# Optimization experiments

Measured on AMD Instinct MI355X. Metric: run time of the kernel, lower is better.

The kernel has to match this reference:

```python
import jax, jax.numpy as jnp
import numpy as np

B, P, K_NB, D, H = 4, 1024, 32, 768, 12
S = P + 1
HD = D // H  # 64

def _ln(x, w, b):
    m = jnp.mean(x, -1, keepdims=True)
    v = jnp.var(x, -1, keepdims=True)
    return (x - m) / jnp.sqrt(v + 1e-5) * w + b

def setup_inputs() -> dict:
    key = jax.random.key(0)
    ks = jax.random.split(key, 8)
    w = lambda k, sh: jax.random.normal(k, sh, jnp.float32) * 0.02
    return {
        'x': jax.random.normal(ks[0], (B, S, D), jnp.float32),
        'routes': jax.random.randint(ks[1], (P, K_NB), 0, P, dtype=jnp.int32),
        'qkv_w': w(ks[2], (D, 3 * D)), 'qkv_b': jnp.zeros((3 * D,), jnp.float32),
        'proj_w': w(ks[3], (D, D)), 'proj_b': jnp.zeros((D,), jnp.float32),
        'ln1_w': jnp.ones((D,), jnp.float32), 'ln1_b': jnp.zeros((D,), jnp.float32),
        'ln2_w': jnp.ones((D,), jnp.float32), 'ln2_b': jnp.zeros((D,), jnp.float32),
        'mlp_w1': w(ks[4], (D, 4 * D)), 'mlp_b1': jnp.zeros((4 * D,), jnp.float32),
        'mlp_w2': w(ks[5], (4 * D, D)), 'mlp_b2': jnp.zeros((D,), jnp.float32),
    }

def reference(x, routes, qkv_w, qkv_b, proj_w, proj_b, ln1_w, ln1_b,
              ln2_w, ln2_b, mlp_w1, mlp_b1, mlp_w2, mlp_b2):
    scale = HD ** -0.5
    xn = _ln(x, ln1_w, ln1_b)
    qkv = (xn @ qkv_w + qkv_b).reshape(B, S, 3, H, HD).transpose(2, 0, 3, 1, 4)
    Q, Kt, V = qkv[0], qkv[1], qkv[2]  # each [B,H,S,HD]
    # CLS token: full dense attention over all S tokens
    sc = jnp.einsum('bhqd,bhkd->bhqk', Q[:, :, :1], Kt) * scale
    oc = jnp.einsum('bhqk,bhkd->bhqd', jax.nn.softmax(sc, -1), V)  # [B,H,1,HD]
    # patch tokens: sparse attention over k routed neighbors
    r = routes + 1  # shift past CLS (buffer routes_shifted)
    Kg = Kt[:, :, r, :]  # [B,H,P,k,HD] gathered keys
    Vg = V[:, :, r, :]   # [B,H,P,k,HD] gathered values
    sp = jnp.einsum('bhpd,bhpkd->bhpk', Q[:, :, 1:], Kg) * scale
    op = jnp.einsum('bhpk,bhpkd->bhpd', jax.nn.softmax(sp, -1), Vg)
    out = jnp.concatenate([oc, op], axis=2).transpose(0, 2, 1, 3).reshape(B, S, D)
    x = x + (out @ proj_w + proj_b)
    h = _ln(x, ln2_w, ln2_b)
    h = jax.nn.gelu(h @ mlp_w1 + mlp_b1, approximate=False) @ mlp_w2 + mlp_b2
    return x + h
```

## Files before the change

### kernel.cpp

```cpp
#include <hip/hip_runtime.h>
#include <hip/hip_bf16.h>

using bf16 = __hip_bfloat16;
using s8v  = __attribute__((ext_vector_type(8))) short;
using f4v  = __attribute__((ext_vector_type(4))) float;

constexpr int B_   = 4;
constexpr int P_   = 1024;
constexpr int KNB  = 32;
constexpr int D_   = 768;
constexpr int H_   = 12;
constexpr int S_   = P_ + 1;
constexpr int M_   = B_ * S_;
constexpr int MPAD = 4224;

#define DEVI static __device__ __forceinline__
#define WAITVM(N) asm volatile("s_waitcnt vmcnt(" #N ")" ::: "memory")
#define MEMFENCE  asm volatile("" ::: "memory")

DEVI float b2f_lo(unsigned u) { return __builtin_bit_cast(float, u << 16); }
DEVI float b2f_hi(unsigned u) { return __builtin_bit_cast(float, u & 0xffff0000u); }
DEVI unsigned short f2bu(float f) {
  return __builtin_bit_cast(unsigned short, __float2bfloat16(f));
}

template<int KK, int NN>
__global__ __launch_bounds__(256)
void wt_conv(const float* __restrict__ W, bf16* __restrict__ Wt) {
  __shared__ float t[32][33];
  int bk = blockIdx.x * 32, bn = blockIdx.y * 32;
  int tx = threadIdx.x & 31, ty = threadIdx.x >> 5;
#pragma unroll
  for (int i = 0; i < 32; i += 8)
    t[ty + i][tx] = W[(size_t)(bk + ty + i) * NN + bn + tx];
  __syncthreads();
#pragma unroll
  for (int i = 0; i < 32; i += 8)
    Wt[(size_t)(bn + ty + i) * KK + bk + tx] = __float2bfloat16(t[tx][ty + i]);
}

__global__ __launch_bounds__(256)
void ln_kernel(const float* __restrict__ x, const float* __restrict__ w,
               const float* __restrict__ b, bf16* __restrict__ out) {
  int row = blockIdx.x;
  const float* xr = x + (size_t)row * D_;
  int t = threadIdx.x;
  float v0 = xr[t], v1 = xr[t + 256], v2 = xr[t + 512];
  float s = v0 + v1 + v2;
  float ss = v0 * v0 + v1 * v1 + v2 * v2;
#pragma unroll
  for (int o = 32; o; o >>= 1) { s += __shfl_xor(s, o); ss += __shfl_xor(ss, o); }
  __shared__ float sm[4], sv[4];
  if ((t & 63) == 0) { sm[t >> 6] = s; sv[t >> 6] = ss; }
  __syncthreads();
  float S = sm[0] + sm[1] + sm[2] + sm[3];
  float SS = sv[0] + sv[1] + sv[2] + sv[3];
  float mean = S * (1.f / D_);
  float var  = SS * (1.f / D_) - mean * mean;
  float inv  = rsqrtf(var + 1e-5f);
  bf16* orow = out + (size_t)row * D_;
  orow[t]       = __float2bfloat16((v0 - mean) * inv * w[t]       + b[t]);
  orow[t + 256] = __float2bfloat16((v1 - mean) * inv * w[t + 256] + b[t + 256]);
  orow[t + 512] = __float2bfloat16((v2 - mean) * inv * w[t + 512] + b[t + 512]);
}

template<int BM, int N, int K, int MODE>
__global__ __launch_bounds__(256)
void gemm_bf16(const bf16* __restrict__ A, const bf16* __restrict__ Bt,
               const float* __restrict__ bias, const float* __restrict__ resid,
               void* __restrict__ dst) {
  constexpr int MR   = BM / 32;
  constexpr int LPS  = BM / 64 + 2;
  constexpr int TN   = N / 128;
  constexpr int NBLK = (MPAD / BM) * TN;
  __shared__ bf16 ldsA[4][BM * 32];
  __shared__ bf16 ldsB[4][128 * 32];

  int bid = blockIdx.x;
  constexpr int NQ = NBLK >> 3, NR = NBLK & 7;
  int xcd = bid & 7, off = bid >> 3;
  int swz = (xcd < NR ? xcd * (NQ + 1) : NR * (NQ + 1) + (xcd - NR) * NQ) + off;
  const int tm = swz / TN, tn = swz % TN;

  const int tid = threadIdx.x;
  const int wid = tid >> 6, lane = tid & 63;
  const int wr = wid >> 1, wc = wid & 1;

  auto stage = [&](int bufi, int step) {
    const int k0 = step * 32;
#pragma unroll
    for (int i = 0; i < BM / 64; ++i) {
      int c = wid * 64 + i * 256 + lane;
      int r = c >> 2, slot = c & 3;
      int gs = slot ^ ((r >> 1) & 3);
      const bf16* ga = A + (size_t)(tm * BM + r) * K + k0 + gs * 8;
      bf16* la = &ldsA[bufi][(wid * 64 + i * 256) * 8];
      __builtin_amdgcn_global_load_lds(
          (__attribute__((address_space(1))) void*)ga,
          (__attribute__((address_space(3))) void*)la, 16, 0, 0);
    }
#pragma unroll
    for (int i = 0; i < 2; ++i) {
      int c = wid * 64 + i * 256 + lane;
      int r = c >> 2, slot = c & 3;
      int gs = slot ^ ((r >> 1) & 3);
      const bf16* ga = Bt + (size_t)(tn * 128 + r) * K + k0 + gs * 8;
      bf16* la = &ldsB[bufi][(wid * 64 + i * 256) * 8];
      __builtin_amdgcn_global_load_lds(
          (__attribute__((address_space(1))) void*)ga,
          (__attribute__((address_space(3))) void*)la, 16, 0, 0);
    }
  };

  f4v acc[MR][4] = {};
  const int nk = K / 32;

  stage(0, 0); stage(1, 1); stage(2, 2);

#pragma unroll 4
  for (int kt = 0; kt < nk; ++kt) {
    const int rem = nk - kt;
    if (rem > 2) {
      if constexpr (LPS == 4) WAITVM(8); else WAITVM(6);
    } else if (rem == 2) {
      if constexpr (LPS == 4) WAITVM(4); else WAITVM(3);
    } else {
      WAITVM(0);
    }
    __builtin_amdgcn_s_barrier();
    MEMFENCE;
    if (kt + 3 < nk) stage((kt + 3) & 3, kt + 3);

    const int cur = kt & 3;
    s8v af[MR], bfv[4];
#pragma unroll
    for (int m = 0; m < MR; ++m) {
      int row = wr * (MR * 16) + m * 16 + (lane & 15);
      int slot = (lane >> 4) ^ ((row >> 1) & 3);
      af[m] = *(const s8v*)&ldsA[cur][row * 32 + slot * 8];
    }
#pragma unroll
    for (int n = 0; n < 4; ++n) {
      int row = wc * 64 + n * 16 + (lane & 15);
      int slot = (lane >> 4) ^ ((row >> 1) & 3);
      bfv[n] = *(const s8v*)&ldsB[cur][row * 32 + slot * 8];
    }
#pragma unroll
    for (int m = 0; m < MR; ++m)
#pragma unroll
      for (int n = 0; n < 4; ++n)
        acc[m][n] = __builtin_amdgcn_mfma_f32_16x16x32_bf16(af[m], bfv[n], acc[m][n], 0, 0, 0);
  }

#pragma unroll
  for (int m = 0; m < MR; ++m)
#pragma unroll
    for (int n = 0; n < 4; ++n)
#pragma unroll
      for (int j = 0; j < 4; ++j) {
        int row = tm * BM + wr * (MR * 16) + m * 16 + (lane >> 4) * 4 + j;
        int col = tn * 128 + wc * 64 + n * 16 + (lane & 15);
        float v = acc[m][n][j];
        if (MODE == 0) {
          if (row < M_) {
            float val = v + bias[col];
            int which = col / 768, rem2 = col % 768;
            int bb = row / S_, s = row % S_;
            ((bf16*)dst)[((size_t)(which * B_ + bb) * S_ + s) * 768 + rem2] =
                __float2bfloat16(val);
          }
        } else if (MODE == 1) {
          if (row < M_) {
            float val = v + bias[col] + resid[(size_t)row * N + col];
            ((float*)dst)[(size_t)row * N + col] = val;
          }
        } else {
          float val = v + bias[col];
          val = 0.5f * val * (1.f + erff(val * 0.70710678f));
          ((bf16*)dst)[(size_t)row * N + col] = __float2bfloat16(val);
        }
      }
}

__global__ __launch_bounds__(256)
void cls_partial(const bf16* __restrict__ QKV, float* __restrict__ part) {
  int bh = blockIdx.x, c = blockIdx.y;
  int b = bh / H_, h = bh % H_;
  const bf16* q  = QKV + ((size_t)(0 * B_ + b) * S_) * D_ + h * 64;
  const bf16* Kr = QKV + ((size_t)(1 * B_ + b) * S_) * D_ + h * 64;
  const bf16* Vr = QKV + ((size_t)(2 * B_ + b) * S_) * D_ + h * 64;
  int k0 = c * 256, kn = (c == 3) ? 257 : 256;
  __shared__ float qf[64];
  __shared__ float sc[257];
  __shared__ float red[4];
  __shared__ float pv[4][64];
  int t = threadIdx.x;
  if (t < 64) qf[t] = __bfloat162float(q[t]);
  __syncthreads();
  for (int kk = t; kk < kn; kk += 256) {
    const uint4* k4 = (const uint4*)(Kr + (size_t)(k0 + kk) * D_);
    float s = 0.f;
#pragma unroll
    for (int i = 0; i < 8; ++i) {
      uint4 kv = k4[i];
      const float* q8 = &qf[i * 8];
      s += b2f_lo(kv.x) * q8[0] + b2f_hi(kv.x) * q8[1]
         + b2f_lo(kv.y) * q8[2] + b2f_hi(kv.y) * q8[3]
         + b2f_lo(kv.z) * q8[4] + b2f_hi(kv.z) * q8[5]
         + b2f_lo(kv.w) * q8[6] + b2f_hi(kv.w) * q8[7];
    }
    sc[kk] = s * 0.125f;
  }
  __syncthreads();
  float mx = -1e30f;
  for (int kk = t; kk < kn; kk += 256) mx = fmaxf(mx, sc[kk]);
#pragma unroll
  for (int o = 32; o; o >>= 1) mx = fmaxf(mx, __shfl_xor(mx, o));
  if ((t & 63) == 0) red[t >> 6] = mx;
  __syncthreads();
  float M = fmaxf(fmaxf(red[0], red[1]), fmaxf(red[2], red[3]));
  __syncthreads();
  float sum = 0.f;
  for (int kk = t; kk < kn; kk += 256) { float e = __expf(sc[kk] - M); sc[kk] = e; sum += e; }
#pragma unroll
  for (int o = 32; o; o >>= 1) sum += __shfl_xor(sum, o);
  if ((t & 63) == 0) red[t >> 6] = sum;
  __syncthreads();
  float L = red[0] + red[1] + red[2] + red[3];
  int d = t & 63, kg = t >> 6;
  float acc = 0.f;
  for (int kk = kg; kk < kn; kk += 4)
    acc += sc[kk] * __bfloat162float(Vr[(size_t)(k0 + kk) * D_ + d]);
  pv[kg][d] = acc;
  __syncthreads();
  float* pp = part + ((size_t)bh * 4 + c) * 68;
  if (t < 64) pp[4 + t] = pv[0][t] + pv[1][t] + pv[2][t] + pv[3][t];
  else if (t == 64) pp[0] = M;
  else if (t == 65) pp[1] = L;
}

__global__ __launch_bounds__(64)
void cls_combine(const float* __restrict__ part, bf16* __restrict__ out) {
  int bh = blockIdx.x, t = threadIdx.x;
  const float* pp = part + (size_t)bh * 4 * 68;
  float m0 = pp[0], m1 = pp[68], m2 = pp[136], m3 = pp[204];
  float M = fmaxf(fmaxf(m0, m1), fmaxf(m2, m3));
  float e0 = __expf(m0 - M), e1 = __expf(m1 - M), e2 = __expf(m2 - M), e3 = __expf(m3 - M);
  float L = pp[1] * e0 + pp[69] * e1 + pp[137] * e2 + pp[205] * e3;
  float o = pp[4 + t] * e0 + pp[72 + t] * e1 + pp[140 + t] * e2 + pp[208 + t] * e3;
  int b = bh / H_, h = bh % H_;
  out[(size_t)(b * S_) * D_ + h * 64 + t] = __float2bfloat16(o / L);
}

__global__ __launch_bounds__(256)
void routed_attn(const bf16* __restrict__ QKV, const int* __restrict__ routes,
                 bf16* __restrict__ out) {
  int unit = blockIdx.x * 4 + (threadIdx.x >> 6);
  int lane = threadIdx.x & 63;
  int h = unit % H_;
  int bp = unit / H_;
  int p = bp % P_, b = bp / P_;

  int k = lane & 31, hi = lane >> 5;
  int r = routes[p * KNB + k] + 1;

  const bf16* Qp = QKV + ((size_t)(0 * B_ + b) * S_ + (p + 1)) * D_ + h * 64 + hi * 32;
  const bf16* Kb = QKV + ((size_t)(1 * B_ + b) * S_) * D_;
  const bf16* Vb = QKV + ((size_t)(2 * B_ + b) * S_) * D_;

  const uint4* q4 = (const uint4*)Qp;
  const uint4* k4 = (const uint4*)(Kb + (size_t)r * D_ + h * 64 + hi * 32);
  float dot = 0.f;
#pragma unroll
  for (int i = 0; i < 4; ++i) {
    uint4 qv = q4[i], kv = k4[i];
    dot += b2f_lo(kv.x) * b2f_lo(qv.x) + b2f_hi(kv.x) * b2f_hi(qv.x)
         + b2f_lo(kv.y) * b2f_lo(qv.y) + b2f_hi(kv.y) * b2f_hi(qv.y)
         + b2f_lo(kv.z) * b2f_lo(qv.z) + b2f_hi(kv.z) * b2f_hi(qv.z)
         + b2f_lo(kv.w) * b2f_lo(qv.w) + b2f_hi(kv.w) * b2f_hi(qv.w);
  }
  dot += __shfl_xor(dot, 32);
  float sc = dot * 0.125f;

  float mx = sc;
#pragma unroll
  for (int o = 16; o; o >>= 1) mx = fmaxf(mx, __shfl_xor(mx, o));
  float w = __expf(sc - mx);
  float sum = w;
#pragma unroll
  for (int o = 16; o; o >>= 1) sum += __shfl_xor(sum, o);
  float inv = 1.f / sum;

  int c = lane & 7, kr0 = lane >> 3;
  float acc[8] = {};
#pragma unroll
  for (int j = 0; j < 4; ++j) {
    int kj = (kr0 & 7) + 8 * j;
    float wj = __shfl(w, kj);
    int rj = __shfl(r, kj);
    uint4 vv = *(const uint4*)(Vb + (size_t)rj * D_ + h * 64 + c * 8);
    acc[0] += wj * b2f_lo(vv.x); acc[1] += wj * b2f_hi(vv.x);
    acc[2] += wj * b2f_lo(vv.y); acc[3] += wj * b2f_hi(vv.y);
    acc[4] += wj * b2f_lo(vv.z); acc[5] += wj * b2f_hi(vv.z);
    acc[6] += wj * b2f_lo(vv.w); acc[7] += wj * b2f_hi(vv.w);
  }
#pragma unroll
  for (int s = 8; s < 64; s <<= 1)
#pragma unroll
    for (int d = 0; d < 8; ++d) acc[d] += __shfl_xor(acc[d], s);

  if (lane < 8) {
    s8v o;
#pragma unroll
    for (int d = 0; d < 8; ++d) o[d] = (short)f2bu(acc[d] * inv);
    *(s8v*)(out + ((size_t)(b * S_ + p + 1)) * D_ + h * 64 + c * 8) = o;
  }
}

extern "C" void kernel_launch(void* const* d_in, const int* in_sizes, int n_in,
                              void* d_out, int out_size, void* d_ws, size_t ws_size,
                              hipStream_t stream) {
  const float* x      = (const float*)d_in[0];
  const int*   routes = (const int*)d_in[1];
  const float* qkv_w  = (const float*)d_in[2];
  const float* qkv_b  = (const float*)d_in[3];
  const float* proj_w = (const float*)d_in[4];
  const float* proj_b = (const float*)d_in[5];
  const float* ln1_w  = (const float*)d_in[6];
  const float* ln1_b  = (const float*)d_in[7];
  const float* ln2_w  = (const float*)d_in[8];
  const float* ln2_b  = (const float*)d_in[9];
  const float* mlp_w1 = (const float*)d_in[10];
  const float* mlp_b1 = (const float*)d_in[11];
  const float* mlp_w2 = (const float*)d_in[12];
  const float* mlp_b2 = (const float*)d_in[13];
  float* out = (float*)d_out;

  bf16* qkvw_t  = (bf16*)d_ws;
  bf16* projw_t = qkvw_t + 2304 * 768;
  bf16* mlpw1_t = projw_t + 768 * 768;
  bf16* mlpw2_t = mlpw1_t + 3072 * 768;
  bf16* xnA     = mlpw2_t + 768 * 3072;
  bf16* qkvbuf  = xnA + (size_t)MPAD * 768;
  bf16* attn    = qkvbuf + (size_t)3 * B_ * S_ * 768;
  bf16* h2      = attn + (size_t)MPAD * 768;
  bf16* g       = xnA;
  float* clsp   = (float*)(attn + (size_t)M_ * 768);

  wt_conv<768, 2304><<<dim3(24, 72), 256, 0, stream>>>(qkv_w, qkvw_t);
  wt_conv<768, 768><<<dim3(24, 24), 256, 0, stream>>>(proj_w, projw_t);
  wt_conv<768, 3072><<<dim3(24, 96), 256, 0, stream>>>(mlp_w1, mlpw1_t);
  wt_conv<3072, 768><<<dim3(96, 24), 256, 0, stream>>>(mlp_w2, mlpw2_t);

  ln_kernel<<<M_, 256, 0, stream>>>(x, ln1_w, ln1_b, xnA);

  gemm_bf16<128, 2304, 768, 0><<<33 * 18, 256, 0, stream>>>(xnA, qkvw_t, qkv_b, nullptr, qkvbuf);

  routed_attn<<<(B_ * P_ * H_) / 4, 256, 0, stream>>>(qkvbuf, routes, attn);
  cls_partial<<<dim3(B_ * H_, 4), 256, 0, stream>>>(qkvbuf, clsp);
  cls_combine<<<B_ * H_, 64, 0, stream>>>(clsp, attn);

  gemm_bf16<64, 768, 768, 1><<<66 * 6, 256, 0, stream>>>(attn, projw_t, proj_b, x, out);

  ln_kernel<<<M_, 256, 0, stream>>>(out, ln2_w, ln2_b, h2);

  gemm_bf16<128, 3072, 768, 2><<<33 * 24, 256, 0, stream>>>(h2, mlpw1_t, mlp_b1, nullptr, g);

  gemm_bf16<64, 768, 3072, 1><<<66 * 6, 256, 0, stream>>>(g, mlpw2_t, mlp_b2, out, out);
}
```

Measured before the change: 361.7 us.

## Split-K the N=768 GEMMs with bf16 partials and a separate reduce kernel

The projection and MLP-down GEMMs (N=768) are split along K into two chunks via blockIdx.y, which doubles the block count to fill more CUs. Each chunk writes bf16 partial sums into freed workspace, and a new reduceK kernel adds bias, residual and both partials. The GEMM pipeline also drops from 4 to 3 LDS buffers, and s_setprio is raised around the MFMA block. The cost is an extra kernel launch, the partial-sum traffic, and extra rounding from storing partials in bf16.

```diff
diff --git a/kernel.cpp b/kernel.cpp
--- a/kernel.cpp
+++ b/kernel.cpp
@@ -20,6 +20,7 @@
 
 DEVI float b2f_lo(unsigned u) { return __builtin_bit_cast(float, u << 16); }
 DEVI float b2f_hi(unsigned u) { return __builtin_bit_cast(float, u & 0xffff0000u); }
+DEVI float bu2f(unsigned short u) { return __builtin_bit_cast(float, (unsigned)u << 16); }
 DEVI unsigned short f2bu(float f) {
   return __builtin_bit_cast(unsigned short, __float2bfloat16(f));
 }
@@ -64,36 +65,36 @@
   orow[t + 512] = __float2bfloat16((v2 - mean) * inv * w[t + 512] + b[t + 512]);
 }
 
-template<int BM, int N, int K, int MODE>
+template<int BM, int N, int KSTRIDE, int KCHUNK, int MODE>
 __global__ __launch_bounds__(256)
 void gemm_bf16(const bf16* __restrict__ A, const bf16* __restrict__ Bt,
-               const float* __restrict__ bias, const float* __restrict__ resid,
-               void* __restrict__ dst) {
+               const float* __restrict__ bias, void* __restrict__ dst) {
   constexpr int MR   = BM / 32;
   constexpr int LPS  = BM / 64 + 2;
   constexpr int TN   = N / 128;
   constexpr int NBLK = (MPAD / BM) * TN;
-  __shared__ bf16 ldsA[4][BM * 32];
-  __shared__ bf16 ldsB[4][128 * 32];
+  __shared__ bf16 ldsA[3][BM * 32];
+  __shared__ bf16 ldsB[3][128 * 32];
 
   int bid = blockIdx.x;
   constexpr int NQ = NBLK >> 3, NR = NBLK & 7;
   int xcd = bid & 7, off = bid >> 3;
   int swz = (xcd < NR ? xcd * (NQ + 1) : NR * (NQ + 1) + (xcd - NR) * NQ) + off;
   const int tm = swz / TN, tn = swz % TN;
+  const int kbase = blockIdx.y * KCHUNK;
 
   const int tid = threadIdx.x;
   const int wid = tid >> 6, lane = tid & 63;
   const int wr = wid >> 1, wc = wid & 1;
 
   auto stage = [&](int bufi, int step) {
-    const int k0 = step * 32;
+    const int k0 = kbase + step * 32;
 #pragma unroll
     for (int i = 0; i < BM / 64; ++i) {
       int c = wid * 64 + i * 256 + lane;
       int r = c >> 2, slot = c & 3;
       int gs = slot ^ ((r >> 1) & 3);
-      const bf16* ga = A + (size_t)(tm * BM + r) * K + k0 + gs * 8;
+      const bf16* ga = A + (size_t)(tm * BM + r) * KSTRIDE + k0 + gs * 8;
       bf16* la = &ldsA[bufi][(wid * 64 + i * 256) * 8];
       __builtin_amdgcn_global_load_lds(
           (__attribute__((address_space(1))) void*)ga,
@@ -104,7 +105,7 @@
       int c = wid * 64 + i * 256 + lane;
       int r = c >> 2, slot = c & 3;
       int gs = slot ^ ((r >> 1) & 3);
-      const bf16* ga = Bt + (size_t)(tn * 128 + r) * K + k0 + gs * 8;
+      const bf16* ga = Bt + (size_t)(tn * 128 + r) * KSTRIDE + k0 + gs * 8;
       bf16* la = &ldsB[bufi][(wid * 64 + i * 256) * 8];
       __builtin_amdgcn_global_load_lds(
           (__attribute__((address_space(1))) void*)ga,
@@ -113,25 +114,22 @@
   };
 
   f4v acc[MR][4] = {};
-  const int nk = K / 32;
-
-  stage(0, 0); stage(1, 1); stage(2, 2);
-
-#pragma unroll 4
+  const int nk = KCHUNK / 32;
+
+  stage(0, 0); stage(1, 1);
+
+#pragma unroll 3
   for (int kt = 0; kt < nk; ++kt) {
-    const int rem = nk - kt;
-    if (rem > 2) {
-      if constexpr (LPS == 4) WAITVM(8); else WAITVM(6);
-    } else if (rem == 2) {
+    if (kt < nk - 1) {
       if constexpr (LPS == 4) WAITVM(4); else WAITVM(3);
     } else {
       WAITVM(0);
     }
     __builtin_amdgcn_s_barrier();
     MEMFENCE;
-    if (kt + 3 < nk) stage((kt + 3) & 3, kt + 3);
-
-    const int cur = kt & 3;
+    if (kt + 2 < nk) stage((kt + 2) % 3, kt + 2);
+
+    const int cur = kt % 3;
     s8v af[MR], bfv[4];
 #pragma unroll
     for (int m = 0; m < MR; ++m) {
@@ -145,11 +143,13 @@
       int slot = (lane >> 4) ^ ((row >> 1) & 3);
       bfv[n] = *(const s8v*)&ldsB[cur][row * 32 + slot * 8];
     }
+    __builtin_amdgcn_s_setprio(1);
 #pragma unroll
     for (int m = 0; m < MR; ++m)
 #pragma unroll
       for (int n = 0; n < 4; ++n)
         acc[m][n] = __builtin_amdgcn_mfma_f32_16x16x32_bf16(af[m], bfv[n], acc[m][n], 0, 0, 0);
+    __builtin_amdgcn_s_setprio(0);
   }
 
 #pragma unroll
@@ -169,17 +169,35 @@
             ((bf16*)dst)[((size_t)(which * B_ + bb) * S_ + s) * 768 + rem2] =
                 __float2bfloat16(val);
           }
-        } else if (MODE == 1) {
+        } else if (MODE == 2) {
           if (row < M_) {
-            float val = v + bias[col] + resid[(size_t)row * N + col];
-            ((float*)dst)[(size_t)row * N + col] = val;
+            float val = v + bias[col];
+            val = 0.5f * val * (1.f + erff(val * 0.70710678f));
+            ((bf16*)dst)[(size_t)row * N + col] = __float2bfloat16(val);
           }
         } else {
-          float val = v + bias[col];
-          val = 0.5f * val * (1.f + erff(val * 0.70710678f));
-          ((bf16*)dst)[(size_t)row * N + col] = __float2bfloat16(val);
+          bf16* p = (bf16*)dst + (size_t)blockIdx.y * MPAD * N;
+          p[(size_t)row * N + col] = __float2bfloat16(v);
         }
       }
+}
+
+template<bool IP>
+__global__ __launch_bounds__(256)
+void reduceK(const bf16* __restrict__ part, const float* __restrict__ src,
+             const float* __restrict__ bias, float* __restrict__ out) {
+  int i = blockIdx.x * 256 + threadIdx.x;
+  ushort4 a = ((const ushort4*)part)[i];
+  ushort4 b = ((const ushort4*)(part + (size_t)MPAD * 768))[i];
+  float4 s = IP ? ((const float4*)out)[i] : ((const float4*)src)[i];
+  int col = (i * 4) % D_;
+  float4 bv = *(const float4*)&bias[col];
+  float4 o;
+  o.x = s.x + bv.x + bu2f(a.x) + bu2f(b.x);
+  o.y = s.y + bv.y + bu2f(a.y) + bu2f(b.y);
+  o.z = s.z + bv.z + bu2f(a.z) + bu2f(b.z);
+  o.w = s.w + bv.w + bu2f(a.w) + bu2f(b.w);
+  ((float4*)out)[i] = o;
 }
 
 __global__ __launch_bounds__(256)
@@ -345,6 +363,8 @@
   bf16* attn    = qkvbuf + (size_t)3 * B_ * S_ * 768;
   bf16* h2      = attn + (size_t)MPAD * 768;
   bf16* g       = xnA;
+  bf16* projp   = xnA;
+  bf16* mlp2p   = attn;
   float* clsp   = (float*)(attn + (size_t)M_ * 768);
 
   wt_conv<768, 2304><<<dim3(24, 72), 256, 0, stream>>>(qkv_w, qkvw_t);
@@ -354,17 +374,19 @@
 
   ln_kernel<<<M_, 256, 0, stream>>>(x, ln1_w, ln1_b, xnA);
 
-  gemm_bf16<128, 2304, 768, 0><<<33 * 18, 256, 0, stream>>>(xnA, qkvw_t, qkv_b, nullptr, qkvbuf);
+  gemm_bf16<128, 2304, 768, 768, 0><<<33 * 18, 256, 0, stream>>>(xnA, qkvw_t, qkv_b, qkvbuf);
 
   routed_attn<<<(B_ * P_ * H_) / 4, 256, 0, stream>>>(qkvbuf, routes, attn);
   cls_partial<<<dim3(B_ * H_, 4), 256, 0, stream>>>(qkvbuf, clsp);
   cls_combine<<<B_ * H_, 64, 0, stream>>>(clsp, attn);
 
-  gemm_bf16<64, 768, 768, 1><<<66 * 6, 256, 0, stream>>>(attn, projw_t, proj_b, x, out);
+  gemm_bf16<64, 768, 768, 384, 3><<<dim3(66 * 6, 2), 256, 0, stream>>>(attn, projw_t, nullptr, projp);
+  reduceK<false><<<(M_ * D_) / 1024, 256, 0, stream>>>(projp, x, proj_b, out);
 
   ln_kernel<<<M_, 256, 0, stream>>>(out, ln2_w, ln2_b, h2);
 
-  gemm_bf16<128, 3072, 768, 2><<<33 * 24, 256, 0, stream>>>(h2, mlpw1_t, mlp_b1, nullptr, g);
-
-  gemm_bf16<64, 768, 3072, 1><<<66 * 6, 256, 0, stream>>>(g, mlpw2_t, mlp_b2, out, out);
-}
+  gemm_bf16<128, 3072, 768, 768, 2><<<33 * 24, 256, 0, stream>>>(h2, mlpw1_t, mlp_b1, g);
+
+  gemm_bf16<64, 768, 3072, 1536, 3><<<dim3(66 * 6, 2), 256, 0, stream>>>(g, mlpw2_t, nullptr, mlp2p);
+  reduceK<true><<<(M_ * D_) / 1024, 256, 0, stream>>>(mlp2p, nullptr, mlp_b2, out);
+}
```

Measured after the change: 342.0 us. -5.4%, faster.
